# Kernel tuning notes

Hardware: AMD Instinct MI355X
Metric: run time of the kernel (lower is better)

## Reference

```python
import jax, jax.numpy as jnp
import numpy as np

B, T, C, HS = 8, 2048, 1024, 128

def setup_inputs() -> dict:
    key = jax.random.key(0)
    kx, kq, kk, kv = jax.random.split(key, 4)
    x = jax.random.normal(kx, (B, T, C), dtype=jnp.float32)
    # torch Linear(C, HS, bias=False): y = x @ W^T with W [HS, C].
    # We store the transposed form [C, HS] and right-multiply (same math).
    scale = 1.0 / np.sqrt(C)  # torch default init scale-ish; exact init irrelevant for correctness
    Wq = jax.random.normal(kq, (C, HS), dtype=jnp.float32) * scale
    Wk = jax.random.normal(kk, (C, HS), dtype=jnp.float32) * scale
    Wv = jax.random.normal(kv, (C, HS), dtype=jnp.float32) * scale
    return {"x": x, "Wq": Wq, "Wk": Wk, "Wv": Wv}

def reference(x, Wq, Wk, Wv):
    Bx, Tx, Cx = x.shape
    q = x @ Wq  # [B, T, HS]
    k = x @ Wk
    v = x @ Wv
    # NOTE: original scales by C**-0.5 where C = n_embd (not head_size)
    wei = jnp.einsum('btd,bsd->bts', q, k) * (Cx ** -0.5)  # [B, T, T]
    causal = jnp.tril(jnp.ones((Tx, Tx), dtype=bool))
    wei = jnp.where(causal, wei, -jnp.inf)
    wei = jax.nn.softmax(wei, axis=-1)
    # dropout rate 0.0 (eval semantics) -> identity
    return jnp.einsum('bts,bsd->btd', wei, v)  # [B, T, HS]
```

## Files before the change

### kernel.cpp

```cpp
#include <hip/hip_runtime.h>
#include <hip/hip_bf16.h>
#include <stdint.h>

typedef float f32x4 __attribute__((ext_vector_type(4)));
typedef float f32x4v __attribute__((ext_vector_type(4)));
typedef short short8 __attribute__((ext_vector_type(8)));
typedef unsigned short u16;
typedef unsigned short u16x8 __attribute__((ext_vector_type(8)));
typedef unsigned short u16x4 __attribute__((ext_vector_type(4)));

#define MFMA16x16x32 __builtin_amdgcn_mfma_f32_16x16x32_bf16

__device__ __forceinline__ u16 f2bf(float f) {
    unsigned int u = __builtin_bit_cast(unsigned int, f);
    u += 0x7fffu + ((u >> 16) & 1u);
    return (u16)(u >> 16);
}

__device__ __forceinline__ void gload_lds16(const void* g, void* l) {
    __builtin_amdgcn_global_load_lds(
        (const __attribute__((address_space(1))) uint32_t*)g,
        (__attribute__((address_space(3))) uint32_t*)l, 16, 0, 0);
}

__device__ __forceinline__ void barrier_lgkm() {
    asm volatile("s_waitcnt lgkmcnt(0)\n\ts_barrier" ::: "memory");
}

__device__ __forceinline__ int z_small(int na) {
    int za = (8 * na + 32) / 33;
    return za < 1 ? 1 : za;
}

__global__ void k_transpose_wf(const float* __restrict__ Wq, const float* __restrict__ Wk,
                               const float* __restrict__ Wv, u16* __restrict__ WTf) {
    int tid  = blockIdx.x * 256 + threadIdx.x;
    int f    = tid >> 6;
    int lane = tid & 63;
    int kt  = f / 48;
    int rem = f % 48;
    int ks  = rem / 24;
    int nc  = rem % 24;
    int col = nc * 16 + (lane & 15);
    int w   = col >> 7, n = col & 127;
    int k0  = kt * 64 + ks * 32 + (lane >> 4) * 8;
    const float* W = (w == 0) ? Wq : ((w == 1) ? Wk : Wv);
    u16x8 v;
#pragma unroll
    for (int j = 0; j < 8; ++j)
        v[j] = f2bf(W[(size_t)(k0 + j) * 128 + n]);
    *(u16x8*)(&WTf[(size_t)tid * 8]) = v;
}

__global__ __launch_bounds__(256) void k_qkv_gemm7(
    const float* __restrict__ x, const u16* __restrict__ WTf,
    u16* __restrict__ qb, u16* __restrict__ kb, u16* __restrict__ vT)
{
    __shared__ u16 la[32 * 64];
    const int tid  = threadIdx.x;
    const int lane = tid & 63, wid = tid >> 6;
    const int lrow = lane & 15, lk = lane >> 4;
    const int m  = blockIdx.x & 511;
    const int nh = blockIdx.x >> 9;
    const int m0 = m * 32;

    const int arow = tid >> 3;
    const int aseg = tid & 7;
    const float* xsrc = x + (size_t)(m0 + arow) * 1024 + aseg * 8;
    const u16* wb = WTf + (size_t)(nh * 12 + wid * 3) * 512 + lane * 8;

    f32x4 acc[2][3];
#pragma unroll
    for (int i = 0; i < 2; ++i)
#pragma unroll
        for (int j = 0; j < 3; ++j) acc[i][j] = (f32x4){0.f, 0.f, 0.f, 0.f};

#define LOADA(s0, s1, ktv)                                                     \
    s0 = *(const f32x4v*)(xsrc + (ktv) * 64);                                  \
    s1 = *(const f32x4v*)(xsrc + (ktv) * 64 + 4);

#define LOADB(dst, ktv)                                                        \
    _Pragma("unroll") for (int ks = 0; ks < 2; ++ks)                           \
    _Pragma("unroll") for (int nf = 0; nf < 3; ++nf)                           \
        dst[ks][nf] = *(const short8*)(wb + (size_t)(((ktv)*2 + ks)*24 + nf) * 512);

#define STOREA(s0, s1)                                                         \
    {   u16x8 v;                                                               \
        v[0]=f2bf(s0[0]); v[1]=f2bf(s0[1]); v[2]=f2bf(s0[2]); v[3]=f2bf(s0[3]); \
        v[4]=f2bf(s1[0]); v[5]=f2bf(s1[1]); v[6]=f2bf(s1[2]); v[7]=f2bf(s1[3]); \
        *(u16x8*)(&la[arow * 64 + ((aseg ^ (arow & 7)) << 3)]) = v; }

#define COMPUTE(bsrc)                                                          \
    _Pragma("unroll") for (int ks = 0; ks < 2; ++ks) {                         \
        short8 af[2];                                                          \
        _Pragma("unroll") for (int mf = 0; mf < 2; ++mf) {                     \
            int row = mf * 16 + lrow;                                          \
            int blk = (ks * 4 + lk) ^ (row & 7);                               \
            af[mf] = *(const short8*)(&la[row * 64 + (blk << 3)]);             \
        }                                                                      \
        _Pragma("unroll") for (int mf = 0; mf < 2; ++mf)                       \
        _Pragma("unroll") for (int nf = 0; nf < 3; ++nf)                       \
            acc[mf][nf] = MFMA16x16x32(af[mf], bsrc[ks][nf], acc[mf][nf], 0, 0, 0); }

    f32x4v a0A, a1A, a0B, a1B;
    short8 bA[2][3], bB[2][3];
    LOADA(a0A, a1A, 0);
    LOADA(a0B, a1B, 1);
    LOADB(bA, 0);
    for (int kt = 0; kt < 16; kt += 2) {
        barrier_lgkm();
        STOREA(a0A, a1A);
        if (kt + 2 < 16) { LOADA(a0A, a1A, kt + 2); }
        LOADB(bB, kt + 1);
        barrier_lgkm();
        COMPUTE(bA);
        barrier_lgkm();
        STOREA(a0B, a1B);
        if (kt + 3 < 16) { LOADA(a0B, a1B, kt + 3); }
        if (kt + 2 < 16) { LOADB(bA, kt + 2); }
        barrier_lgkm();
        COMPUTE(bB);
    }
#undef LOADA
#undef LOADB
#undef STOREA
#undef COMPUTE

#pragma unroll
    for (int nf = 0; nf < 3; ++nf) {
        const int gc   = nh * 192 + wid * 48 + nf * 16 + lrow;
        const int wsel = gc >> 7;
        const int col  = gc & 127;
#pragma unroll
        for (int mf = 0; mf < 2; ++mf) {
            const int row0 = m0 + mf * 16 + lk * 4;
            if (wsel == 0) {
#pragma unroll
                for (int jj = 0; jj < 4; ++jj)
                    qb[(size_t)(row0 + jj) * 128 + col] = f2bf(acc[mf][nf][jj]);
            } else if (wsel == 1) {
#pragma unroll
                for (int jj = 0; jj < 4; ++jj)
                    kb[(size_t)(row0 + jj) * 128 + col] = f2bf(acc[mf][nf][jj]);
            } else {
                const int bb = row0 >> 11, t0 = row0 & 2047;
                u16x4 v;
#pragma unroll
                for (int jj = 0; jj < 4; ++jj) v[jj] = f2bf(acc[mf][nf][jj]);
                *(u16x4*)(&vT[((size_t)bb * 128 + col) * 2048 + t0]) = v;
            }
        }
    }
}

__global__ __launch_bounds__(256) void k_flash6(
    const u16* __restrict__ qb, const u16* __restrict__ kb, const u16* __restrict__ vT,
    float* __restrict__ po, float* __restrict__ pm, float* __restrict__ pl)
{
    __shared__ u16 k_lds[64 * 128];
    __shared__ u16 v_lds[128 * 64];
    __shared__ u16 p_lds[4 * 16 * 64];
    const int tid  = threadIdx.x;
    const int lane = tid & 63, wid = tid >> 6;
    const int lrow = lane & 15, lk = lane >> 4;
    const int bx = blockIdx.x;
    const int b  = bx & 7;
    const int p  = (bx >> 3) & 15;
    const int z  = bx >> 7;

    const int na = p + 1;
    const int za = z_small(na);
    int qt, n, k, Z;
    if (z < za) { qt = p;      n = na;     k = z;      Z = za;     }
    else        { qt = 31 - p; n = 32 - p; k = z - za; Z = 8 - za; }
    const int t0 = (k * n) / Z;
    const int t1 = ((k + 1) * n) / Z;

    const int qrow0 = qt * 64;
    short8 qf[4];
    {
        const u16* qp = qb + ((size_t)b * 2048 + qrow0 + wid * 16 + lrow) * 128;
#pragma unroll
        for (int ks = 0; ks < 4; ++ks) qf[ks] = *(const short8*)(qp + ks * 32 + lk * 8);
    }
    f32x4 of[8];
#pragma unroll
    for (int i = 0; i < 8; ++i) of[i] = (f32x4){0.f, 0.f, 0.f, 0.f};
    float mrun[4], lsum[4];
#pragma unroll
    for (int j = 0; j < 4; ++j) { mrun[j] = -1e30f; lsum[j] = 0.f; }

    const u16* kbase = kb + (size_t)b * 2048 * 128;
    const u16* vbase = vT + (size_t)b * 128 * 2048;
    u16* pw = p_lds + wid * (16 * 64);

    for (int t = t0; t < t1; ++t) {
        const int kv0 = t << 6;
        __syncthreads();
#pragma unroll
        for (int i = 0; i < 4; ++i) {
            int c = tid + i * 256;
            int row = c >> 4, blk = c & 15;
            gload_lds16(kbase + (size_t)(kv0 + row) * 128 + ((blk ^ (row & 7)) << 3),
                        &k_lds[c * 8]);
        }
#pragma unroll
        for (int i = 0; i < 4; ++i) {
            int c = tid + i * 256;
            int row = c >> 3, blk = c & 7;
            gload_lds16(vbase + (size_t)row * 2048 + kv0 + ((blk ^ (row & 7)) << 3),
                        &v_lds[c * 8]);
        }
        __syncthreads();

        f32x4 sf[4];
#pragma unroll
        for (int nf = 0; nf < 4; ++nf) sf[nf] = (f32x4){0.f, 0.f, 0.f, 0.f};
#pragma unroll
        for (int ks = 0; ks < 4; ++ks)
#pragma unroll
            for (int nf = 0; nf < 4; ++nf) {
                int row = nf * 16 + lrow;
                int blk = (ks * 4 + lk) ^ (row & 7);
                short8 bfr = *(const short8*)(&k_lds[row * 128 + (blk << 3)]);
                sf[nf] = MFMA16x16x32(qf[ks], bfr, sf[nf], 0, 0, 0);
            }

        const bool diag = (t == n - 1);
#pragma unroll
        for (int nf = 0; nf < 4; ++nf)
#pragma unroll
            for (int jj = 0; jj < 4; ++jj) {
                float s = sf[nf][jj] * 0.03125f;
                if (diag && (nf * 16 + lrow > wid * 16 + lk * 4 + jj)) s = -1e30f;
                sf[nf][jj] = s;
            }
        float mt[4];
#pragma unroll
        for (int jj = 0; jj < 4; ++jj)
            mt[jj] = fmaxf(fmaxf(sf[0][jj], sf[1][jj]), fmaxf(sf[2][jj], sf[3][jj]));
#pragma unroll
        for (int off = 1; off < 16; off <<= 1)
#pragma unroll
            for (int jj = 0; jj < 4; ++jj)
                mt[jj] = fmaxf(mt[jj], __shfl_xor(mt[jj], off));
        bool small = true;
#pragma unroll
        for (int jj = 0; jj < 4; ++jj) small = small && (mt[jj] <= mrun[jj] + 8.f);
        if (!__all(small)) {
#pragma unroll
            for (int jj = 0; jj < 4; ++jj) {
                float mnew = fmaxf(mrun[jj], mt[jj]);
                float sc   = __expf(mrun[jj] - mnew);
                mrun[jj]   = mnew;
                lsum[jj]  *= sc;
#pragma unroll
                for (int df = 0; df < 8; ++df) of[df][jj] *= sc;
            }
        }
        float rs[4] = {0.f, 0.f, 0.f, 0.f};
#pragma unroll
        for (int nf = 0; nf < 4; ++nf)
#pragma unroll
            for (int jj = 0; jj < 4; ++jj) {
                float e = __expf(sf[nf][jj] - mrun[jj]);
                sf[nf][jj] = e;
                rs[jj] += e;
            }
#pragma unroll
        for (int off = 1; off < 16; off <<= 1)
#pragma unroll
            for (int jj = 0; jj < 4; ++jj)
                rs[jj] += __shfl_xor(rs[jj], off);
#pragma unroll
        for (int jj = 0; jj < 4; ++jj) lsum[jj] += rs[jj];

#pragma unroll
        for (int nf = 0; nf < 4; ++nf)
#pragma unroll
            for (int jj = 0; jj < 4; ++jj) {
                int row = lk * 4 + jj;
                int col = nf * 16 + lrow;
                pw[row * 64 + (((col >> 3) ^ (row & 7)) << 3) + (col & 7)] = f2bf(sf[nf][jj]);
            }
        asm volatile("s_waitcnt lgkmcnt(0)" ::: "memory");
        __builtin_amdgcn_sched_barrier(0);
        short8 paf[2];
#pragma unroll
        for (int ks2 = 0; ks2 < 2; ++ks2) {
            int blk = (ks2 * 4 + lk) ^ (lrow & 7);
            paf[ks2] = *(const short8*)(&pw[lrow * 64 + (blk << 3)]);
        }
#pragma unroll
        for (int ks2 = 0; ks2 < 2; ++ks2)
#pragma unroll
            for (int df = 0; df < 8; ++df) {
                int row = df * 16 + lrow;
                int blk = (ks2 * 4 + lk) ^ (row & 7);
                short8 vf = *(const short8*)(&v_lds[row * 64 + (blk << 3)]);
                of[df] = MFMA16x16x32(paf[ks2], vf, of[df], 0, 0, 0);
            }
    }

    float* poslab = po + (size_t)bx * (64 * 128);
#pragma unroll
    for (int df = 0; df < 8; ++df)
#pragma unroll
        for (int jj = 0; jj < 4; ++jj)
            poslab[(size_t)(wid * 16 + lk * 4 + jj) * 128 + df * 16 + lrow] = of[df][jj];
    if (lrow == 0) {
#pragma unroll
        for (int jj = 0; jj < 4; ++jj) {
            pm[(size_t)bx * 64 + wid * 16 + lk * 4 + jj] = mrun[jj];
            pl[(size_t)bx * 64 + wid * 16 + lk * 4 + jj] = lsum[jj];
        }
    }
}

__global__ __launch_bounds__(256) void k_combine(
    const float* __restrict__ po, const float* __restrict__ pm, const float* __restrict__ pl,
    float* __restrict__ out)
{
    const int row  = blockIdx.x * 4 + (threadIdx.x >> 6);
    const int lane = threadIdx.x & 63;
    const int b  = row >> 11;
    const int t  = row & 2047;
    const int qt = t >> 6;
    const int r  = t & 63;

    const int p  = (qt < 16) ? qt : 31 - qt;
    const int za = z_small(p + 1);
    const int zlo = (qt < 16) ? 0 : za;
    const int zhi = (qt < 16) ? za : 8;

    float M = -1e30f;
    for (int z = zlo; z < zhi; ++z)
        M = fmaxf(M, pm[(size_t)(b + 8 * p + 128 * z) * 64 + r]);
    float den = 0.f, a0 = 0.f, a1 = 0.f;
    for (int z = zlo; z < zhi; ++z) {
        const int bxp = b + 8 * p + 128 * z;
        const float w = __expf(pm[(size_t)bxp * 64 + r] - M);
        den += w * pl[(size_t)bxp * 64 + r];
        const float* slab = po + ((size_t)bxp * 64 + r) * 128;
        a0 += w * slab[lane];
        a1 += w * slab[lane + 64];
    }
    const float inv = 1.f / den;
    out[(size_t)row * 128 + lane]      = a0 * inv;
    out[(size_t)row * 128 + lane + 64] = a1 * inv;
}

extern "C" void kernel_launch(void* const* d_in, const int* in_sizes, int n_in,
                              void* d_out, int out_size, void* d_ws, size_t ws_size,
                              hipStream_t stream) {
    const float* x  = (const float*)d_in[0];
    const float* Wq = (const float*)d_in[1];
    const float* Wk = (const float*)d_in[2];
    const float* Wv = (const float*)d_in[3];
    float* out = (float*)d_out;

    char* ws = (char*)d_ws;
    u16*   qb  = (u16*)(ws);
    u16*   kb  = (u16*)(ws + (size_t)4  * 1048576);
    u16*   vT  = (u16*)(ws + (size_t)8  * 1048576);
    u16*   WTf = (u16*)(ws + (size_t)12 * 1048576);
    float* po  = (float*)(ws + (size_t)13 * 1048576);
    float* pm  = (float*)(ws + (size_t)47 * 1048576);
    float* pl  = (float*)(ws + (size_t)48 * 1048576);

    k_transpose_wf<<<192, 256, 0, stream>>>(Wq, Wk, Wv, WTf);
    k_qkv_gemm7<<<1024, 256, 0, stream>>>(x, WTf, qb, kb, vT);
    k_flash6<<<1024, 256, 0, stream>>>(qb, kb, vT, po, pm, pl);
    k_combine<<<4096, 256, 0, stream>>>(po, pm, pl, out);
}
```

Measured before the change: 81.71 us.

## Retile QKV GEMM to 64-row blocks with LDS-staged, double-buffered weights

The QKV projection kernel now has each 512-thread block compute 64 rows against all 384 output columns. Previously 1024 blocks each computed 32 rows by 192 columns and read weight fragments straight from global memory into registers. Weight tiles are now staged into double-buffered LDS with asynchronous global-to-LDS loads, and the A tile is double-buffered as well, so fewer barriers are needed per step and weight loads overlap compute. This cuts redundant global weight reads and halves x re-reads. In exchange it uses much more LDS (about 112 KB), has fewer blocks (256), and relies on hand-tuned vmcnt waits.

```diff
diff --git a/kernel.cpp b/kernel.cpp
--- a/kernel.cpp
+++ b/kernel.cpp
@@ -21,10 +21,6 @@
     __builtin_amdgcn_global_load_lds(
         (const __attribute__((address_space(1))) uint32_t*)g,
         (__attribute__((address_space(3))) uint32_t*)l, 16, 0, 0);
-}
-
-__device__ __forceinline__ void barrier_lgkm() {
-    asm volatile("s_waitcnt lgkmcnt(0)\n\ts_barrier" ::: "memory");
 }
 
 __device__ __forceinline__ int z_small(int na) {
@@ -52,88 +48,107 @@
     *(u16x8*)(&WTf[(size_t)tid * 8]) = v;
 }
 
-__global__ __launch_bounds__(256) void k_qkv_gemm7(
+__global__ __launch_bounds__(512) void k_qkv_gemm8(
     const float* __restrict__ x, const u16* __restrict__ WTf,
     u16* __restrict__ qb, u16* __restrict__ kb, u16* __restrict__ vT)
 {
-    __shared__ u16 la[32 * 64];
+    __shared__ u16 abuf[2][64 * 64];
+    __shared__ u16 bbuf[2][384 * 64];
     const int tid  = threadIdx.x;
     const int lane = tid & 63, wid = tid >> 6;
+    const int wr = wid >> 2, wc = wid & 3;
     const int lrow = lane & 15, lk = lane >> 4;
-    const int m  = blockIdx.x & 511;
-    const int nh = blockIdx.x >> 9;
-    const int m0 = m * 32;
+    const int m0 = blockIdx.x * 64;
 
     const int arow = tid >> 3;
     const int aseg = tid & 7;
     const float* xsrc = x + (size_t)(m0 + arow) * 1024 + aseg * 8;
-    const u16* wb = WTf + (size_t)(nh * 12 + wid * 3) * 512 + lane * 8;
-
-    f32x4 acc[2][3];
+
+    f32x4 acc[2][6];
 #pragma unroll
     for (int i = 0; i < 2; ++i)
 #pragma unroll
-        for (int j = 0; j < 3; ++j) acc[i][j] = (f32x4){0.f, 0.f, 0.f, 0.f};
+        for (int j = 0; j < 6; ++j) acc[i][j] = (f32x4){0.f, 0.f, 0.f, 0.f};
 
 #define LOADA(s0, s1, ktv)                                                     \
     s0 = *(const f32x4v*)(xsrc + (ktv) * 64);                                  \
     s1 = *(const f32x4v*)(xsrc + (ktv) * 64 + 4);
 
-#define LOADB(dst, ktv)                                                        \
-    _Pragma("unroll") for (int ks = 0; ks < 2; ++ks)                           \
-    _Pragma("unroll") for (int nf = 0; nf < 3; ++nf)                           \
-        dst[ks][nf] = *(const short8*)(wb + (size_t)(((ktv)*2 + ks)*24 + nf) * 512);
-
-#define STOREA(s0, s1)                                                         \
+#define STOREA(buf, s0, s1)                                                    \
     {   u16x8 v;                                                               \
         v[0]=f2bf(s0[0]); v[1]=f2bf(s0[1]); v[2]=f2bf(s0[2]); v[3]=f2bf(s0[3]); \
         v[4]=f2bf(s1[0]); v[5]=f2bf(s1[1]); v[6]=f2bf(s1[2]); v[7]=f2bf(s1[3]); \
-        *(u16x8*)(&la[arow * 64 + ((aseg ^ (arow & 7)) << 3)]) = v; }
-
-#define COMPUTE(bsrc)                                                          \
+        *(u16x8*)(&buf[arow * 64 + ((aseg ^ (arow & 7)) << 3)]) = v; }
+
+#define ISSUEB(buf, ktv)                                                       \
+    {   const u16* bsrc = WTf + (size_t)(ktv) * 24576;                         \
+        _Pragma("unroll") for (int i = 0; i < 6; ++i) {                        \
+            int c = tid + i * 512;                                             \
+            gload_lds16(bsrc + c * 8, &buf[c * 8]);                            \
+        } }
+
+#define COMPUTE(ab, bb)                                                        \
     _Pragma("unroll") for (int ks = 0; ks < 2; ++ks) {                         \
         short8 af[2];                                                          \
         _Pragma("unroll") for (int mf = 0; mf < 2; ++mf) {                     \
-            int row = mf * 16 + lrow;                                          \
+            int row = wr * 32 + mf * 16 + lrow;                                \
             int blk = (ks * 4 + lk) ^ (row & 7);                               \
-            af[mf] = *(const short8*)(&la[row * 64 + (blk << 3)]);             \
+            af[mf] = *(const short8*)(&ab[row * 64 + (blk << 3)]);             \
         }                                                                      \
-        _Pragma("unroll") for (int mf = 0; mf < 2; ++mf)                       \
-        _Pragma("unroll") for (int nf = 0; nf < 3; ++nf)                       \
-            acc[mf][nf] = MFMA16x16x32(af[mf], bsrc[ks][nf], acc[mf][nf], 0, 0, 0); }
+        _Pragma("unroll") for (int nf = 0; nf < 6; ++nf) {                     \
+            short8 bfr = *(const short8*)(&bb[(ks * 24 + wc * 6 + nf) * 512 + lane * 8]); \
+            _Pragma("unroll") for (int mf = 0; mf < 2; ++mf)                   \
+                acc[mf][nf] = MFMA16x16x32(af[mf], bfr, acc[mf][nf], 0, 0, 0); \
+        } }
+
+#define WAITBAR()                                                              \
+    asm volatile("s_waitcnt vmcnt(2) lgkmcnt(0)\n\ts_barrier" ::: "memory");   \
+    __builtin_amdgcn_sched_barrier(0);
 
     f32x4v a0A, a1A, a0B, a1B;
-    short8 bA[2][3], bB[2][3];
     LOADA(a0A, a1A, 0);
     LOADA(a0B, a1B, 1);
-    LOADB(bA, 0);
+    STOREA(abuf[0], a0A, a1A);
+    ISSUEB(bbuf[0], 0);
+    LOADA(a0A, a1A, 2);
+    WAITBAR();
+
     for (int kt = 0; kt < 16; kt += 2) {
-        barrier_lgkm();
-        STOREA(a0A, a1A);
-        if (kt + 2 < 16) { LOADA(a0A, a1A, kt + 2); }
-        LOADB(bB, kt + 1);
-        barrier_lgkm();
-        COMPUTE(bA);
-        barrier_lgkm();
-        STOREA(a0B, a1B);
-        if (kt + 3 < 16) { LOADA(a0B, a1B, kt + 3); }
-        if (kt + 2 < 16) { LOADB(bA, kt + 2); }
-        barrier_lgkm();
-        COMPUTE(bB);
+        {
+            const int ktn = (kt + 1 < 16) ? kt + 1 : 15;
+            ISSUEB(bbuf[1], ktn);
+            __builtin_amdgcn_sched_barrier(0);
+            COMPUTE(abuf[0], bbuf[0]);
+            STOREA(abuf[1], a0B, a1B);
+            const int kp = (kt + 3 < 16) ? kt + 3 : 15;
+            LOADA(a0B, a1B, kp);
+            WAITBAR();
+        }
+        {
+            const int ktn = (kt + 2 < 16) ? kt + 2 : 15;
+            ISSUEB(bbuf[0], ktn);
+            __builtin_amdgcn_sched_barrier(0);
+            COMPUTE(abuf[1], bbuf[1]);
+            STOREA(abuf[0], a0A, a1A);
+            const int kp = (kt + 4 < 16) ? kt + 4 : 15;
+            LOADA(a0A, a1A, kp);
+            WAITBAR();
+        }
     }
 #undef LOADA
-#undef LOADB
 #undef STOREA
+#undef ISSUEB
 #undef COMPUTE
-
-#pragma unroll
-    for (int nf = 0; nf < 3; ++nf) {
-        const int gc   = nh * 192 + wid * 48 + nf * 16 + lrow;
+#undef WAITBAR
+
+#pragma unroll
+    for (int nf = 0; nf < 6; ++nf) {
+        const int gc   = wc * 96 + nf * 16 + lrow;
         const int wsel = gc >> 7;
         const int col  = gc & 127;
 #pragma unroll
         for (int mf = 0; mf < 2; ++mf) {
-            const int row0 = m0 + mf * 16 + lk * 4;
+            const int row0 = m0 + wr * 32 + mf * 16 + lk * 4;
             if (wsel == 0) {
 #pragma unroll
                 for (int jj = 0; jj < 4; ++jj)
@@ -369,7 +384,7 @@
     float* pl  = (float*)(ws + (size_t)48 * 1048576);
 
     k_transpose_wf<<<192, 256, 0, stream>>>(Wq, Wk, Wv, WTf);
-    k_qkv_gemm7<<<1024, 256, 0, stream>>>(x, WTf, qb, kb, vT);
+    k_qkv_gemm8<<<256, 512, 0, stream>>>(x, WTf, qb, kb, vT);
     k_flash6<<<1024, 256, 0, stream>>>(qb, kb, vT, po, pm, pl);
     k_combine<<<4096, 256, 0, stream>>>(po, pm, pl, out);
 }
```

Result: faster. 78.86 us (-3.5%).
